# Kernel tuning notes

Hardware: AMD Instinct MI355X
Metric: run time of the kernel (lower is better)

## Reference

```python
import jax, jax.numpy as jnp
import numpy as np

KH, KW, F = 2, 3, 32  # ConvLSTM kernel and filters


def _conv(x, w, padding):
    # x: [B,H,W,Cin], w: [kh,kw,Cin,Cout]
    return jax.lax.conv_general_dilated(
        x, w, (1, 1), padding, dimension_numbers=("NHWC", "HWIO", "NHWC"))


def _hard_sigmoid(x):
    # Keras hard_sigmoid: clip(0.2*x + 0.5, 0, 1)
    return jnp.clip(0.2 * x + 0.5, 0.0, 1.0)


def convlstm2d(x, W, U, b):
    # Keras ConvLSTM2D, padding='valid' on input conv, 'same' on recurrent conv,
    # activation=relu, recurrent_activation=hard_sigmoid, return_sequences=True.
    B, T, H, Wd, C = x.shape
    f = W.shape[-1] // 4
    Ho, Wo = H - KH + 1, Wd - KW + 1
    h0 = jnp.zeros((B, Ho, Wo, f), x.dtype)

    def step(carry, xt):
        h, c = carry
        z = _conv(xt, W, "VALID") + _conv(h, U, "SAME") + b
        zi, zf, zc, zo = jnp.split(z, 4, axis=-1)  # gate order i,f,c,o
        i = _hard_sigmoid(zi)
        fg = _hard_sigmoid(zf)
        c_new = fg * c + i * jax.nn.relu(zc)
        h_new = _hard_sigmoid(zo) * jax.nn.relu(c_new)
        return (h_new, c_new), h_new

    xs = jnp.moveaxis(x, 1, 0)  # [T,B,H,W,C]
    _, hs = jax.lax.scan(step, (h0, h0), xs)
    return jnp.moveaxis(hs, 0, 1)  # [B,T,Ho,Wo,F]


def maxpool3d(x):
    # MaxPooling3D pool_size=(1,2,2) over (T,H,W) of [B,T,H,W,C]
    return jax.lax.reduce_window(x, -jnp.inf, jax.lax.max,
                                 (1, 1, 2, 2, 1), (1, 1, 2, 2, 1), "VALID")


def setup_inputs() -> dict:
    key = jax.random.key(0)
    ks = jax.random.split(key, 12)
    s = 0.05
    B, T, H, Wd, C = 16, 12, 48, 48, 3
    x = jax.random.normal(ks[0], (B, T, H, Wd, C), jnp.float32)
    W1 = jax.random.normal(ks[1], (KH, KW, C, 4 * F), jnp.float32) * s
    U1 = jax.random.normal(ks[2], (KH, KW, F, 4 * F), jnp.float32) * s
    b1 = jnp.zeros((4 * F,), jnp.float32)
    W2 = jax.random.normal(ks[3], (KH, KW, F, 4 * F), jnp.float32) * s
    U2 = jax.random.normal(ks[4], (KH, KW, F, 4 * F), jnp.float32) * s
    b2 = jnp.zeros((4 * F,), jnp.float32)
    # after two convlstms: 48->47->46 (H), 48->46->44 (W); pool -> 23x22
    flat = T * 23 * 22 * F  # 194304
    Wd1 = jax.random.normal(ks[5], (flat, 10), jnp.float32) * 0.01
    bd1 = jnp.zeros((10,), jnp.float32)
    Wd2 = jax.random.normal(ks[6], (10, 1), jnp.float32) * 0.1
    bd2 = jnp.zeros((1,), jnp.float32)
    return {"x": x, "W1": W1, "U1": U1, "b1": b1, "W2": W2, "U2": U2,
            "b2": b2, "Wd1": Wd1, "bd1": bd1, "Wd2": Wd2, "bd2": bd2}


def reference(x, W1, U1, b1, W2, U2, b2, Wd1, bd1, Wd2, bd2):
    h1 = convlstm2d(x, W1, U1, b1)
    h2 = convlstm2d(h1, W2, U2, b2)
    p = maxpool3d(h2)            # dropout = identity at inference
    f = p.reshape(p.shape[0], -1)
    d1 = f @ Wd1 + bd1
    return d1 @ Wd2 + bd2        # [B,1]
```

## Files before the change

kernel.cpp:

```cpp
#include <hip/hip_runtime.h>
#include <math.h>

#define NB 16
#define TT 12
#define H1 47
#define W1D 46
#define H2 46
#define W2D 44

typedef short short8v __attribute__((ext_vector_type(8)));
typedef float floatx4 __attribute__((ext_vector_type(4)));

__device__ __forceinline__ short f2bf(float x) {
    unsigned u = __float_as_uint(x);
    u = (u + 0x7FFFu + ((u >> 16) & 1u)) >> 16;
    return (short)u;
}
__device__ __forceinline__ float bf2f(short s) {
    return __uint_as_float(((unsigned)(unsigned short)s) << 16);
}
__device__ __forceinline__ float hsig(float z) {
    return fminf(fmaxf(0.2f * z + 0.5f, 0.f), 1.f);
}

__global__ __launch_bounds__(256) void convert_x(const float* __restrict__ x,
                                                 short* __restrict__ xbf, int n) {
    int i = blockIdx.x * 256 + threadIdx.x;
    if (i < n) xbf[i] = f2bf(x[i]);
}

__global__ __launch_bounds__(256) void transform_w(
    const float* __restrict__ W1s, const float* __restrict__ U1s,
    const float* __restrict__ W2s, const float* __restrict__ U2s,
    short* __restrict__ Bt1, short* __restrict__ Bt2)
{
    int idx = blockIdx.x * 256 + threadIdx.x;
    int layer2 = idx >= 28672;
    int i = layer2 ? idx - 28672 : idx;
    int ci = i & 31, j = (i >> 5) & 15, g = (i >> 9) & 3, fh = (i >> 11) & 1, c = i >> 12;
    int col = g * 32 + fh * 16 + j;
    float v = 0.f;
    if (!layer2) {
        if (c == 0) {
            if (ci < 18) { int kk = ci / 3, cc = ci - kk * 3; v = W1s[(kk * 3 + cc) * 128 + col]; }
        } else {
            v = U1s[((c - 1) * 32 + ci) * 128 + col];
        }
    } else {
        if (c < 6) v = W2s[(c * 32 + ci) * 128 + col];
        else       v = U2s[((c - 6) * 32 + ci) * 128 + col];
    }
    (layer2 ? Bt2 : Bt1)[i] = f2bf(v);
}

template<int LAYER>
__device__ __forceinline__ void step_body(
    const short* __restrict__ xin,
    const short* __restrict__ hprev,
    const short* __restrict__ Bt,
    const float* __restrict__ bias,
    float* __restrict__ cstp,
    short* __restrict__ hnext,
    short* __restrict__ pool, int t2, int t1, int first,
    int b, int y0, int x0, short* ldsrec, short* ldsaux)
{
    constexpr int Ho   = (LAYER == 1) ? H1 : H2;
    constexpr int Wo   = (LAYER == 1) ? W1D : W2D;
    constexpr int NCH  = (LAYER == 1) ? 7 : 12;
    constexpr int REC0 = (LAYER == 1) ? 1 : 6;
    constexpr int IBS  = (LAYER == 1) ? (TT * 48 * 48 * 3) : (H1 * W1D * 32);
    constexpr int HBS  = Ho * Wo * 32;

    const int tid = threadIdx.x;
    const int lane = tid & 63;
    const int fh = tid >> 6;
    const int tx = lane & 15, q = lane >> 4;
    const short8v z8 = (short8v)0;

    {
        const short* hb0 = hprev + b * HBS;
        for (int i = tid; i < 360; i += 128) {
            int p = i >> 2, c4 = i & 3;
            int row = p / 18, col = p - row * 18;
            int y = y0 + row, x = x0 + col - 1;
            short8v v = z8;
            if (!first && y < Ho && (unsigned)x < (unsigned)Wo)
                v = *(const short8v*)(hb0 + (y * Wo + x) * 32 + c4 * 8);
            *(short8v*)&ldsrec[p * 40 + c4 * 8] = v;
        }
    }

    if (LAYER == 1) {
        const short* xb0 = xin + b * IBS + t1 * 6912;
        for (int i = tid; i < 64 * 32; i += 128) {
            int m = i >> 5, k = i & 31;
            short v = 0;
            if (k < 18) {
                int kk = k / 3, cc = k - kk * 3;
                int ky = (kk >= 3) ? 1 : 0, kx = kk - ky * 3;
                int ys = y0 + (m >> 4) + ky; if (ys > 47) ys = 47;
                int xs = x0 + (m & 15) + kx; if (xs > 47) xs = 47;
                v = xb0[(ys * 48 + xs) * 3 + cc];
            }
            ldsaux[m * 40 + k] = v;
        }
    } else {
        const short* ib0 = xin + b * IBS;
        for (int i = tid; i < 360; i += 128) {
            int p = i >> 2, c4 = i & 3;
            int row = p / 18, col = p - row * 18;
            int ys = y0 + row; if (ys > H1 - 1) ys = H1 - 1;
            int xs = x0 + col;
            short8v v = *(const short8v*)(ib0 + (ys * W1D + xs) * 32 + c4 * 8);
            *(short8v*)&ldsaux[p * 40 + c4 * 8] = v;
        }
    }
    __syncthreads();

    const short* Btl = Bt + fh * 2048 + tx * 32 + q * 8;
    floatx4 acc[4][4] = {};

#pragma unroll
    for (int c = 0; c < NCH; ++c) {
        short8v bf4[4], af[4];
#pragma unroll
        for (int g = 0; g < 4; ++g)
            bf4[g] = *(const short8v*)(Btl + c * 4096 + g * 512);

        if (LAYER == 1 && c == 0) {
#pragma unroll
            for (int a = 0; a < 4; ++a)
                af[a] = *(const short8v*)&ldsaux[(a * 16 + tx) * 40 + q * 8];
        } else if (LAYER == 2 && c < REC0) {
            int ky = (c >= 3) ? 1 : 0, kx = c - ky * 3;
#pragma unroll
            for (int a = 0; a < 4; ++a)
                af[a] = *(const short8v*)&ldsaux[(((a + ky) * 18 + tx + kx)) * 40 + q * 8];
        } else {
            int kk = c - REC0;
            int ky = (kk >= 3) ? 1 : 0, kx = kk - ky * 3;
#pragma unroll
            for (int a = 0; a < 4; ++a)
                af[a] = *(const short8v*)&ldsrec[(((a + ky) * 18 + tx + kx)) * 40 + q * 8];
        }
#pragma unroll
        for (int a = 0; a < 4; ++a)
#pragma unroll
            for (int g = 0; g < 4; ++g)
                acc[a][g] = __builtin_amdgcn_mfma_f32_16x16x32_bf16(af[a], bf4[g], acc[a][g], 0, 0, 0);
    }

    const int f = fh * 16 + tx;
    const float bi = bias[f], bfv = bias[32 + f], bcv = bias[64 + f], bov = bias[96 + f];
    float* cme = cstp + tid * 16;
    float hv[4][4];
#pragma unroll
    for (int a = 0; a < 4; ++a) {
        int y = y0 + a;
        bool yok = y < Ho;
        floatx4 cold;
        if (first) { cold[0] = cold[1] = cold[2] = cold[3] = 0.f; }
        else         cold = *(floatx4*)(cme + a * 4);
        floatx4 cnew;
#pragma unroll
        for (int r = 0; r < 4; ++r) {
            int xe = x0 + q * 4 + r;
            float ig = hsig(acc[a][0][r] + bi);
            float fg = hsig(acc[a][1][r] + bfv);
            float gg = fmaxf(acc[a][2][r] + bcv, 0.f);
            float og = hsig(acc[a][3][r] + bov);
            float cn = fg * cold[r] + ig * gg;
            cnew[r] = cn;
            float hn = 0.f;
            if (yok && xe < Wo) {
                short hb = f2bf(og * fmaxf(cn, 0.f));
                hnext[b * HBS + (y * Wo + xe) * 32 + f] = hb;
                hn = bf2f(hb);
            }
            hv[a][r] = hn;
        }
        *(floatx4*)(cme + a * 4) = cnew;
    }

    if (LAYER == 2) {
#pragma unroll
        for (int ap = 0; ap < 2; ++ap) {
            int py = y0 / 2 + ap;
#pragma unroll
            for (int rp = 0; rp < 2; ++rp) {
                int px = x0 / 2 + q * 2 + rp;
                if (py < 23 && px < 22) {
                    float m = fmaxf(fmaxf(hv[2 * ap][2 * rp],     hv[2 * ap][2 * rp + 1]),
                                    fmaxf(hv[2 * ap + 1][2 * rp], hv[2 * ap + 1][2 * rp + 1]));
                    pool[(size_t)b * 194304 + ((t2 * 23 + py) * 22 + px) * 32 + f] = f2bf(m);
                }
            }
        }
    }
}

__global__ __launch_bounds__(128, 3) void fused_step(
    const short* __restrict__ xbf,
    const short* __restrict__ h1r, short* __restrict__ h1w,
    const short* __restrict__ h2r, short* __restrict__ h2w,
    const short* __restrict__ Bt1, const short* __restrict__ Bt2,
    const float* __restrict__ b1, const float* __restrict__ b2,
    float* __restrict__ c1, float* __restrict__ c2,
    short* __restrict__ pool, int t2, int t1,
    int do1, int do2, int first1, int first2)
{
    __shared__ short lds[7200];
    int gid  = blockIdx.x;
    int layer = gid & 1;
    int b     = (gid >> 1) & 15;
    int t36   = gid >> 5;
    int y0 = (t36 / 3) * 4;
    int x0 = (t36 % 3) * 16;

    if (layer == 0) {
        if (!do1) return;
        float* cstp = c1 + (size_t)(b * 36 + t36) * 2048;
        step_body<1>(xbf, h1r, Bt1, b1, cstp, h1w, nullptr, 0, t1, first1,
                     b, y0, x0, lds, lds + 3600);
    } else {
        if (!do2) return;
        float* cstp = c2 + (size_t)(b * 36 + t36) * 2048;
        step_body<2>(h1r, h2r, Bt2, b2, cstp, h2w, pool, t2, 0, first2,
                     b, y0, x0, lds, lds + 3600);
    }
}

__global__ __launch_bounds__(256) void gemv_kernel(
    const short* __restrict__ p, const float* __restrict__ Wd1, float* __restrict__ d1p)
{
    int grp = blockIdx.y;
    int kc = blockIdx.x;
    int k0 = kc * 3036;
    float part[8][10];
#pragma unroll
    for (int bb = 0; bb < 8; bb++)
#pragma unroll
        for (int j = 0; j < 10; j++) part[bb][j] = 0.f;

    for (int k = k0 + threadIdx.x; k < k0 + 3036; k += 256) {
        const float* wr = Wd1 + (size_t)k * 10;
        float wv[10];
#pragma unroll
        for (int j = 0; j < 10; j++) wv[j] = wr[j];
#pragma unroll
        for (int bb = 0; bb < 8; bb++) {
            float m = bf2f(p[(size_t)(grp * 8 + bb) * 194304 + k]);
#pragma unroll
            for (int j = 0; j < 10; j++) part[bb][j] = fmaf(m, wv[j], part[bb][j]);
        }
    }
    __shared__ float red[8][10][4];
    int lane = threadIdx.x & 63, wv2 = threadIdx.x >> 6;
#pragma unroll
    for (int bb = 0; bb < 8; bb++)
#pragma unroll
        for (int j = 0; j < 10; j++) {
            float v = part[bb][j];
            for (int off = 32; off > 0; off >>= 1) v += __shfl_down(v, off);
            if (lane == 0) red[bb][j][wv2] = v;
        }
    __syncthreads();
    if (threadIdx.x < 80) {
        int bb = threadIdx.x / 10, j = threadIdx.x % 10;
        d1p[(kc * 2 + grp) * 80 + bb * 10 + j] =
            red[bb][j][0] + red[bb][j][1] + red[bb][j][2] + red[bb][j][3];
    }
}

__global__ void final_dense(const float* __restrict__ d1p, const float* __restrict__ bd1,
                            const float* __restrict__ Wd2, const float* __restrict__ bd2,
                            float* __restrict__ out)
{
    __shared__ float dj[16][10];
    int tid = threadIdx.x;
    if (tid < 160) {
        int b = tid / 10, j = tid % 10, grp = b >> 3, bb = b & 7;
        float s = 0.f;
        for (int kc = 0; kc < 64; kc++)
            s += d1p[(kc * 2 + grp) * 80 + bb * 10 + j];
        dj[b][j] = s + bd1[j];
    }
    __syncthreads();
    if (tid < NB) {
        float s = bd2[0];
#pragma unroll
        for (int j = 0; j < 10; j++) s += dj[tid][j] * Wd2[j];
        out[tid] = s;
    }
}

extern "C" void kernel_launch(void* const* d_in, const int* in_sizes, int n_in,
                              void* d_out, int out_size, void* d_ws, size_t ws_size,
                              hipStream_t stream)
{
    const float* x   = (const float*)d_in[0];
    const float* W1s = (const float*)d_in[1];
    const float* U1s = (const float*)d_in[2];
    const float* b1  = (const float*)d_in[3];
    const float* W2s = (const float*)d_in[4];
    const float* U2s = (const float*)d_in[5];
    const float* b2  = (const float*)d_in[6];
    const float* Wd1 = (const float*)d_in[7];
    const float* bd1 = (const float*)d_in[8];
    const float* Wd2 = (const float*)d_in[9];
    const float* bd2 = (const float*)d_in[10];
    float* out = (float*)d_out;

    const int H1N = NB * H1 * W1D * 32;
    const int H2N = NB * H2 * W2D * 32;
    const int SLF = 32, SLB = 8192;
    const int SPAN1 = SLF + H1N + SLB;
    const int SPAN2 = SLF + H2N + SLB;
    const int CPL   = 16 * 36 * 2048;

    short* Bt1 = (short*)d_ws;
    short* Bt2 = Bt1 + 28672;
    short* xbf = Bt2 + 49152;
    short* p   = xbf + 1327104;
    short* hr  = p + 3108864;
    short* h1a = hr + SLF;
    short* h1b = hr + SPAN1 + SLF;
    short* h2a = hr + 2 * SPAN1 + SLF;
    short* h2b = hr + 2 * SPAN1 + SPAN2 + SLF;
    float* c1  = (float*)(hr + 2 * SPAN1 + 2 * SPAN2);
    float* c2  = c1 + CPL;
    float* d1p = c2 + CPL;

    convert_x<<<(1327104 + 255) / 256, 256, 0, stream>>>(x, xbf, 1327104);
    transform_w<<<304, 256, 0, stream>>>(W1s, U1s, W2s, U2s, Bt1, Bt2);

    for (int s = 0; s <= TT; s++) {
        short*       h1w = (s & 1) ? h1b : h1a;
        const short* h1r = (s & 1) ? h1a : h1b;
        short*       h2w = (s & 1) ? h2a : h2b;
        const short* h2r = (s & 1) ? h2b : h2a;
        fused_step<<<dim3(1152), 128, 0, stream>>>(
            xbf, h1r, h1w, h2r, h2w, Bt1, Bt2, b1, b2, c1, c2,
            p, s - 1, (s < TT ? s : 0),
            (int)(s < TT), (int)(s >= 1), (int)(s == 0), (int)(s == 1));
    }

    gemv_kernel<<<dim3(64, 2), 256, 0, stream>>>(p, Wd1, d1p);
    final_dense<<<1, 192, 0, stream>>>(d1p, bd1, Wd2, bd2, out);
}
```

Measured before the change: 311.9 us.

## Process two batch samples per block to reuse weight fragments across MFMAs

Each block now handles two batch elements for the same spatial tile, so every loaded B-weight fragment feeds twice as many MFMAs. The grid halves from 1152 to 576 blocks and LDS doubles to hold both samples' input and recurrent tiles. Occupancy hint drops from 3 to 2 blocks per CU to fit the doubled accumulators. The goal is to cut global and L2 weight traffic per MFMA, at the cost of more register pressure and fewer blocks to spread across the CUs.

```diff
diff --git a/kernel.cpp b/kernel.cpp
--- a/kernel.cpp
+++ b/kernel.cpp
@@ -59,10 +59,10 @@
     const short* __restrict__ hprev,
     const short* __restrict__ Bt,
     const float* __restrict__ bias,
-    float* __restrict__ cstp,
+    float* __restrict__ cbase,
     short* __restrict__ hnext,
     short* __restrict__ pool, int t2, int t1, int first,
-    int b, int y0, int x0, short* ldsrec, short* ldsaux)
+    int b0, int t36, int y0, int x0, short* lds)
 {
     constexpr int Ho   = (LAYER == 1) ? H1 : H2;
     constexpr int Wo   = (LAYER == 1) ? W1D : W2D;
@@ -77,8 +77,13 @@
     const int tx = lane & 15, q = lane >> 4;
     const short8v z8 = (short8v)0;
 
-    {
-        const short* hb0 = hprev + b * HBS;
+    short* ldsrec = lds;
+    short* ldsaux = lds + 7200;
+
+#pragma unroll
+    for (int bb = 0; bb < 2; ++bb) {
+        const short* hb0 = hprev + (b0 + bb) * HBS;
+        short* dst = ldsrec + bb * 3600;
         for (int i = tid; i < 360; i += 128) {
             int p = i >> 2, c4 = i & 3;
             int row = p / 18, col = p - row * 18;
@@ -86,120 +91,141 @@
             short8v v = z8;
             if (!first && y < Ho && (unsigned)x < (unsigned)Wo)
                 v = *(const short8v*)(hb0 + (y * Wo + x) * 32 + c4 * 8);
-            *(short8v*)&ldsrec[p * 40 + c4 * 8] = v;
+            *(short8v*)&dst[p * 40 + c4 * 8] = v;
         }
     }
 
     if (LAYER == 1) {
-        const short* xb0 = xin + b * IBS + t1 * 6912;
-        for (int i = tid; i < 64 * 32; i += 128) {
-            int m = i >> 5, k = i & 31;
-            short v = 0;
-            if (k < 18) {
-                int kk = k / 3, cc = k - kk * 3;
-                int ky = (kk >= 3) ? 1 : 0, kx = kk - ky * 3;
-                int ys = y0 + (m >> 4) + ky; if (ys > 47) ys = 47;
-                int xs = x0 + (m & 15) + kx; if (xs > 47) xs = 47;
-                v = xb0[(ys * 48 + xs) * 3 + cc];
+#pragma unroll
+        for (int bb = 0; bb < 2; ++bb) {
+            const short* xb0 = xin + (b0 + bb) * IBS + t1 * 6912;
+            short* dst = ldsaux + bb * 3600;
+            for (int i = tid; i < 64 * 32; i += 128) {
+                int m = i >> 5, k = i & 31;
+                short v = 0;
+                if (k < 18) {
+                    int kk = k / 3, cc = k - kk * 3;
+                    int ky = (kk >= 3) ? 1 : 0, kx = kk - ky * 3;
+                    int ys = y0 + (m >> 4) + ky; if (ys > 47) ys = 47;
+                    int xs = x0 + (m & 15) + kx; if (xs > 47) xs = 47;
+                    v = xb0[(ys * 48 + xs) * 3 + cc];
+                }
+                dst[m * 40 + k] = v;
             }
-            ldsaux[m * 40 + k] = v;
         }
     } else {
-        const short* ib0 = xin + b * IBS;
-        for (int i = tid; i < 360; i += 128) {
-            int p = i >> 2, c4 = i & 3;
-            int row = p / 18, col = p - row * 18;
-            int ys = y0 + row; if (ys > H1 - 1) ys = H1 - 1;
-            int xs = x0 + col;
-            short8v v = *(const short8v*)(ib0 + (ys * W1D + xs) * 32 + c4 * 8);
-            *(short8v*)&ldsaux[p * 40 + c4 * 8] = v;
+#pragma unroll
+        for (int bb = 0; bb < 2; ++bb) {
+            const short* ib0 = xin + (b0 + bb) * IBS;
+            short* dst = ldsaux + bb * 3600;
+            for (int i = tid; i < 360; i += 128) {
+                int p = i >> 2, c4 = i & 3;
+                int row = p / 18, col = p - row * 18;
+                int ys = y0 + row; if (ys > H1 - 1) ys = H1 - 1;
+                int xs = x0 + col;
+                short8v v = *(const short8v*)(ib0 + (ys * W1D + xs) * 32 + c4 * 8);
+                *(short8v*)&dst[p * 40 + c4 * 8] = v;
+            }
         }
     }
     __syncthreads();
 
     const short* Btl = Bt + fh * 2048 + tx * 32 + q * 8;
-    floatx4 acc[4][4] = {};
+    floatx4 acc[2][4][4] = {};
 
 #pragma unroll
     for (int c = 0; c < NCH; ++c) {
-        short8v bf4[4], af[4];
+        short8v bf4[4], af[2][4];
 #pragma unroll
         for (int g = 0; g < 4; ++g)
             bf4[g] = *(const short8v*)(Btl + c * 4096 + g * 512);
 
         if (LAYER == 1 && c == 0) {
 #pragma unroll
-            for (int a = 0; a < 4; ++a)
-                af[a] = *(const short8v*)&ldsaux[(a * 16 + tx) * 40 + q * 8];
+            for (int bb = 0; bb < 2; ++bb)
+#pragma unroll
+                for (int a = 0; a < 4; ++a)
+                    af[bb][a] = *(const short8v*)&ldsaux[bb * 3600 + (a * 16 + tx) * 40 + q * 8];
         } else if (LAYER == 2 && c < REC0) {
             int ky = (c >= 3) ? 1 : 0, kx = c - ky * 3;
 #pragma unroll
-            for (int a = 0; a < 4; ++a)
-                af[a] = *(const short8v*)&ldsaux[(((a + ky) * 18 + tx + kx)) * 40 + q * 8];
+            for (int bb = 0; bb < 2; ++bb)
+#pragma unroll
+                for (int a = 0; a < 4; ++a)
+                    af[bb][a] = *(const short8v*)&ldsaux[bb * 3600 + ((a + ky) * 18 + tx + kx) * 40 + q * 8];
         } else {
             int kk = c - REC0;
             int ky = (kk >= 3) ? 1 : 0, kx = kk - ky * 3;
 #pragma unroll
+            for (int bb = 0; bb < 2; ++bb)
+#pragma unroll
+                for (int a = 0; a < 4; ++a)
+                    af[bb][a] = *(const short8v*)&ldsrec[bb * 3600 + ((a + ky) * 18 + tx + kx) * 40 + q * 8];
+        }
+#pragma unroll
+        for (int bb = 0; bb < 2; ++bb)
+#pragma unroll
             for (int a = 0; a < 4; ++a)
-                af[a] = *(const short8v*)&ldsrec[(((a + ky) * 18 + tx + kx)) * 40 + q * 8];
-        }
-#pragma unroll
-        for (int a = 0; a < 4; ++a)
-#pragma unroll
-            for (int g = 0; g < 4; ++g)
-                acc[a][g] = __builtin_amdgcn_mfma_f32_16x16x32_bf16(af[a], bf4[g], acc[a][g], 0, 0, 0);
+#pragma unroll
+                for (int g = 0; g < 4; ++g)
+                    acc[bb][a][g] = __builtin_amdgcn_mfma_f32_16x16x32_bf16(
+                        af[bb][a], bf4[g], acc[bb][a][g], 0, 0, 0);
     }
 
     const int f = fh * 16 + tx;
     const float bi = bias[f], bfv = bias[32 + f], bcv = bias[64 + f], bov = bias[96 + f];
-    float* cme = cstp + tid * 16;
-    float hv[4][4];
-#pragma unroll
-    for (int a = 0; a < 4; ++a) {
-        int y = y0 + a;
-        bool yok = y < Ho;
-        floatx4 cold;
-        if (first) { cold[0] = cold[1] = cold[2] = cold[3] = 0.f; }
-        else         cold = *(floatx4*)(cme + a * 4);
-        floatx4 cnew;
-#pragma unroll
-        for (int r = 0; r < 4; ++r) {
-            int xe = x0 + q * 4 + r;
-            float ig = hsig(acc[a][0][r] + bi);
-            float fg = hsig(acc[a][1][r] + bfv);
-            float gg = fmaxf(acc[a][2][r] + bcv, 0.f);
-            float og = hsig(acc[a][3][r] + bov);
-            float cn = fg * cold[r] + ig * gg;
-            cnew[r] = cn;
-            float hn = 0.f;
-            if (yok && xe < Wo) {
-                short hb = f2bf(og * fmaxf(cn, 0.f));
-                hnext[b * HBS + (y * Wo + xe) * 32 + f] = hb;
-                hn = bf2f(hb);
+#pragma unroll
+    for (int bb = 0; bb < 2; ++bb) {
+        float* cme = cbase + (size_t)((b0 + bb) * 36 + t36) * 2048 + tid * 16;
+        float hv[4][4];
+#pragma unroll
+        for (int a = 0; a < 4; ++a) {
+            int y = y0 + a;
+            bool yok = y < Ho;
+            floatx4 cold;
+            if (first) { cold[0] = cold[1] = cold[2] = cold[3] = 0.f; }
+            else         cold = *(floatx4*)(cme + a * 4);
+            floatx4 cnew;
+#pragma unroll
+            for (int r = 0; r < 4; ++r) {
+                int xe = x0 + q * 4 + r;
+                float ig = hsig(acc[bb][a][0][r] + bi);
+                float fg = hsig(acc[bb][a][1][r] + bfv);
+                float gg = fmaxf(acc[bb][a][2][r] + bcv, 0.f);
+                float og = hsig(acc[bb][a][3][r] + bov);
+                float cn = fg * cold[r] + ig * gg;
+                cnew[r] = cn;
+                float hn = 0.f;
+                if (yok && xe < Wo) {
+                    short hb = f2bf(og * fmaxf(cn, 0.f));
+                    hnext[(b0 + bb) * HBS + (y * Wo + xe) * 32 + f] = hb;
+                    hn = bf2f(hb);
+                }
+                hv[a][r] = hn;
             }
-            hv[a][r] = hn;
-        }
-        *(floatx4*)(cme + a * 4) = cnew;
-    }
-
-    if (LAYER == 2) {
-#pragma unroll
-        for (int ap = 0; ap < 2; ++ap) {
-            int py = y0 / 2 + ap;
-#pragma unroll
-            for (int rp = 0; rp < 2; ++rp) {
-                int px = x0 / 2 + q * 2 + rp;
-                if (py < 23 && px < 22) {
-                    float m = fmaxf(fmaxf(hv[2 * ap][2 * rp],     hv[2 * ap][2 * rp + 1]),
-                                    fmaxf(hv[2 * ap + 1][2 * rp], hv[2 * ap + 1][2 * rp + 1]));
-                    pool[(size_t)b * 194304 + ((t2 * 23 + py) * 22 + px) * 32 + f] = f2bf(m);
+            *(floatx4*)(cme + a * 4) = cnew;
+        }
+
+        if (LAYER == 2) {
+#pragma unroll
+            for (int ap = 0; ap < 2; ++ap) {
+                int py = y0 / 2 + ap;
+#pragma unroll
+                for (int rp = 0; rp < 2; ++rp) {
+                    int px = x0 / 2 + q * 2 + rp;
+                    if (py < 23 && px < 22) {
+                        float m = fmaxf(fmaxf(hv[2 * ap][2 * rp],     hv[2 * ap][2 * rp + 1]),
+                                        fmaxf(hv[2 * ap + 1][2 * rp], hv[2 * ap + 1][2 * rp + 1]));
+                        pool[(size_t)(b0 + bb) * 194304 +
+                             ((t2 * 23 + py) * 22 + px) * 32 + f] = f2bf(m);
+                    }
                 }
             }
         }
     }
 }
 
-__global__ __launch_bounds__(128, 3) void fused_step(
+__global__ __launch_bounds__(128, 2) void fused_step(
     const short* __restrict__ xbf,
     const short* __restrict__ h1r, short* __restrict__ h1w,
     const short* __restrict__ h2r, short* __restrict__ h2w,
@@ -209,24 +235,22 @@
     short* __restrict__ pool, int t2, int t1,
     int do1, int do2, int first1, int first2)
 {
-    __shared__ short lds[7200];
+    __shared__ short lds[14400];
     int gid  = blockIdx.x;
     int layer = gid & 1;
-    int b     = (gid >> 1) & 15;
-    int t36   = gid >> 5;
+    int b0    = ((gid >> 1) & 7) * 2;
+    int t36   = gid >> 4;
     int y0 = (t36 / 3) * 4;
     int x0 = (t36 % 3) * 16;
 
     if (layer == 0) {
         if (!do1) return;
-        float* cstp = c1 + (size_t)(b * 36 + t36) * 2048;
-        step_body<1>(xbf, h1r, Bt1, b1, cstp, h1w, nullptr, 0, t1, first1,
-                     b, y0, x0, lds, lds + 3600);
+        step_body<1>(xbf, h1r, Bt1, b1, c1, h1w, nullptr, 0, t1, first1,
+                     b0, t36, y0, x0, lds);
     } else {
         if (!do2) return;
-        float* cstp = c2 + (size_t)(b * 36 + t36) * 2048;
-        step_body<2>(h1r, h2r, Bt2, b2, cstp, h2w, pool, t2, 0, first2,
-                     b, y0, x0, lds, lds + 3600);
+        step_body<2>(h1r, h2r, Bt2, b2, c2, h2w, pool, t2, 0, first2,
+                     b0, t36, y0, x0, lds);
     }
 }
 
@@ -339,7 +363,7 @@
         const short* h1r = (s & 1) ? h1a : h1b;
         short*       h2w = (s & 1) ? h2a : h2b;
         const short* h2r = (s & 1) ? h2b : h2a;
-        fused_step<<<dim3(1152), 128, 0, stream>>>(
+        fused_step<<<dim3(576), 128, 0, stream>>>(
             xbf, h1r, h1w, h2r, h2w, Bt1, Bt2, b1, b2, c1, c2,
             p, s - 1, (s < TT ? s : 0),
             (int)(s < TT), (int)(s >= 1), (int)(s == 0), (int)(s == 1));
```

Measured after the change: 353.5 us. 13.3% more time.
